# Performance work log

Measured on AMD Instinct MI355X. Metric: run time of the kernel, lower is better.

## Reference

```python
import jax, jax.numpy as jnp
import numpy as np

M_SLOTS, H, W = 10, 88, 88
B, C = 32, 256

def _xavier_normal(key, shape):
    # torch.nn.init.xavier_normal_ for a 3D tensor [M,H,W]:
    # fan_in = H*W (prod of dims after first? torch: fan_in = shape[1]*receptive, fan_out = shape[0]*receptive)
    # For a 3D tensor torch treats dim1=H as fan dims with receptive field W:
    fan_in = shape[1] * shape[2]
    fan_out = shape[0] * shape[2]
    std = float(np.sqrt(2.0 / (fan_in + fan_out)))
    return jax.random.normal(key, shape, dtype=jnp.float32) * std

def setup_inputs() -> dict:
    key = jax.random.key(0)
    kx, km = jax.random.split(key)
    x = jax.random.normal(kx, (B, C, H, W), dtype=jnp.float32)
    mem = _xavier_normal(km, (M_SLOTS, H, W))
    return {"x": x, "mem": mem}

def reference(x, mem):
    # score[b,c,m] = sum_hw x[b,c,h,w] * mem[m,h,w]
    score = jnp.einsum('bchw,mhw->bcm', x, mem)
    score = jax.nn.softmax(score, axis=-1)
    # value[b,c,h,w] = sum_m score[b,c,m] * mem[m,h,w]
    value = jnp.einsum('bcm,mhw->bchw', score, mem)
    return value
```

## Files before the change

### kernel.cpp

```cpp
#include <hip/hip_runtime.h>


#define RROWS   4
#define NM      10
#define NVEC    1936
#define THREADS 256

typedef float f32x4 __attribute__((ext_vector_type(4)));

__global__ __launch_bounds__(THREADS)
void memaug_kernel(const float* __restrict__ x,
                   const float* __restrict__ mem,
                   float* __restrict__ out)
{
    const int tid = threadIdx.x;
    const long r0 = (long)blockIdx.x * RROWS;

    const f32x4* __restrict__ m4  = (const f32x4*)mem;
    const f32x4* __restrict__ xr  = (const f32x4*)x + r0 * NVEC;
    f32x4* __restrict__ orow      = (f32x4*)out + r0 * NVEC;

    float acc[RROWS][NM];
#pragma unroll
    for (int j = 0; j < RROWS; ++j)
#pragma unroll
        for (int m = 0; m < NM; ++m) acc[j][m] = 0.f;

    for (int iv = tid; iv < NVEC; iv += THREADS) {
        f32x4 xv[RROWS];
#pragma unroll
        for (int j = 0; j < RROWS; ++j)
            xv[j] = xr[j * NVEC + iv];
        f32x4 mv[NM];
#pragma unroll
        for (int m = 0; m < NM; ++m)
            mv[m] = m4[m * NVEC + iv];
#pragma unroll
        for (int m = 0; m < NM; ++m) {
#pragma unroll
            for (int j = 0; j < RROWS; ++j) {
                acc[j][m] += xv[j].x * mv[m].x + xv[j].y * mv[m].y
                           + xv[j].z * mv[m].z + xv[j].w * mv[m].w;
            }
        }
    }

#pragma unroll
    for (int j = 0; j < RROWS; ++j)
#pragma unroll
        for (int m = 0; m < NM; ++m) {
            float v = acc[j][m];
#pragma unroll
            for (int off = 32; off > 0; off >>= 1)
                v += __shfl_xor(v, off, 64);
            acc[j][m] = v;
        }

    __shared__ float red[4][RROWS][NM];
    __shared__ float prob[RROWS][NM];

    const int wave = tid >> 6;
    const int lane = tid & 63;
    if (lane == 0) {
#pragma unroll
        for (int j = 0; j < RROWS; ++j)
#pragma unroll
            for (int m = 0; m < NM; ++m) red[wave][j][m] = acc[j][m];
    }
    __syncthreads();

    if (tid < RROWS) {
        const int j = tid;
        float s[NM];
        float mx = -1e30f;
#pragma unroll
        for (int m = 0; m < NM; ++m) {
            s[m] = red[0][j][m] + red[1][j][m] + red[2][j][m] + red[3][j][m];
            mx = fmaxf(mx, s[m]);
        }
        float sum = 0.f;
#pragma unroll
        for (int m = 0; m < NM; ++m) { s[m] = expf(s[m] - mx); sum += s[m]; }
        const float inv = 1.f / sum;
#pragma unroll
        for (int m = 0; m < NM; ++m) prob[j][m] = s[m] * inv;
    }
    __syncthreads();

    float p[RROWS][NM];
#pragma unroll
    for (int j = 0; j < RROWS; ++j)
#pragma unroll
        for (int m = 0; m < NM; ++m) p[j][m] = prob[j][m];

    for (int iv = tid; iv < NVEC; iv += THREADS) {
        f32x4 mv[NM];
#pragma unroll
        for (int m = 0; m < NM; ++m)
            mv[m] = m4[m * NVEC + iv];

        f32x4 ov[RROWS];
#pragma unroll
        for (int j = 0; j < RROWS; ++j) ov[j] = (f32x4)(0.f);
#pragma unroll
        for (int m = 0; m < NM; ++m) {
#pragma unroll
            for (int j = 0; j < RROWS; ++j) {
                ov[j].x += p[j][m] * mv[m].x;
                ov[j].y += p[j][m] * mv[m].y;
                ov[j].z += p[j][m] * mv[m].z;
                ov[j].w += p[j][m] * mv[m].w;
            }
        }
#pragma unroll
        for (int j = 0; j < RROWS; ++j)
            __builtin_nontemporal_store(ov[j], &orow[j * NVEC + iv]);
    }
}

extern "C" void kernel_launch(void* const* d_in, const int* in_sizes, int n_in,
                              void* d_out, int out_size, void* d_ws, size_t ws_size,
                              hipStream_t stream) {
    const float* x   = (const float*)d_in[0];
    const float* mem = (const float*)d_in[1];
    float* out       = (float*)d_out;

    const int rows   = 32 * 256;
    const int blocks = rows / RROWS;

    memaug_kernel<<<blocks, THREADS, 0, stream>>>(x, mem, out);
}
```

Baseline: 88.45 us.

## Assign rows per wave and add per-chunk block barriers to keep waves in lockstep

Each wave now owns two rows and reduces across the full row on its own, so the shared-memory reduction and softmax barriers are gone. A block covers eight rows, and each of the four waves loads the same mem chunk at the same time. A __syncthreads after every chunk keeps the waves aligned so those shared mem reads can hit in cache together. The cost is a barrier on every iteration and a tail guard in the last chunk.

Result: slower. 106.7 us (+20.7%).

```diff
diff --git a/kernel.cpp b/kernel.cpp
--- a/kernel.cpp
+++ b/kernel.cpp
@@ -1,9 +1,12 @@
 #include <hip/hip_runtime.h>
 
 
-#define RROWS   4
+#define RPW     2
+#define NWAVES  4
+#define ROWS_PB (RPW * NWAVES)
 #define NM      10
 #define NVEC    1936
+#define NCHUNK  31
 #define THREADS 256
 
 typedef float f32x4 __attribute__((ext_vector_type(4)));
@@ -13,40 +16,50 @@
                    const float* __restrict__ mem,
                    float* __restrict__ out)
 {
-    const int tid = threadIdx.x;
-    const long r0 = (long)blockIdx.x * RROWS;
+    const int tid  = threadIdx.x;
+    const int lane = tid & 63;
+    const int wv   = tid >> 6;
+    const long rowbase = (long)blockIdx.x * ROWS_PB + (long)wv * RPW;
 
-    const f32x4* __restrict__ m4  = (const f32x4*)mem;
-    const f32x4* __restrict__ xr  = (const f32x4*)x + r0 * NVEC;
-    f32x4* __restrict__ orow      = (f32x4*)out + r0 * NVEC;
+    const f32x4* __restrict__ m4 = (const f32x4*)mem;
+    const f32x4* __restrict__ xr = (const f32x4*)x + rowbase * NVEC;
+    f32x4* __restrict__ orow     = (f32x4*)out + rowbase * NVEC;
 
-    float acc[RROWS][NM];
+    float acc[RPW][NM];
 #pragma unroll
-    for (int j = 0; j < RROWS; ++j)
+    for (int j = 0; j < RPW; ++j)
 #pragma unroll
         for (int m = 0; m < NM; ++m) acc[j][m] = 0.f;
 
-    for (int iv = tid; iv < NVEC; iv += THREADS) {
-        f32x4 xv[RROWS];
+    for (int c = 0; c < NCHUNK; ++c) {
+        const int iv = c * 64 + lane;
+        const bool ok = iv < NVEC;
+
+        f32x4 xv[RPW], mv[NM];
+        if (ok) {
 #pragma unroll
-        for (int j = 0; j < RROWS; ++j)
-            xv[j] = xr[j * NVEC + iv];
-        f32x4 mv[NM];
+            for (int j = 0; j < RPW; ++j)
+                xv[j] = xr[j * NVEC + iv];
 #pragma unroll
-        for (int m = 0; m < NM; ++m)
-            mv[m] = m4[m * NVEC + iv];
+            for (int m = 0; m < NM; ++m)
+                mv[m] = m4[m * NVEC + iv];
+        } else {
+#pragma unroll
+            for (int j = 0; j < RPW; ++j) xv[j] = (f32x4)(0.f);
+        }
 #pragma unroll
         for (int m = 0; m < NM; ++m) {
 #pragma unroll
-            for (int j = 0; j < RROWS; ++j) {
+            for (int j = 0; j < RPW; ++j) {
                 acc[j][m] += xv[j].x * mv[m].x + xv[j].y * mv[m].y
                            + xv[j].z * mv[m].z + xv[j].w * mv[m].w;
             }
         }
+        __syncthreads();
     }
 
 #pragma unroll
-    for (int j = 0; j < RROWS; ++j)
+    for (int j = 0; j < RPW; ++j)
 #pragma unroll
         for (int m = 0; m < NM; ++m) {
             float v = acc[j][m];
@@ -56,65 +69,48 @@
             acc[j][m] = v;
         }
 
-    __shared__ float red[4][RROWS][NM];
-    __shared__ float prob[RROWS][NM];
-
-    const int wave = tid >> 6;
-    const int lane = tid & 63;
-    if (lane == 0) {
+    float p[RPW][NM];
 #pragma unroll
-        for (int j = 0; j < RROWS; ++j)
-#pragma unroll
-            for (int m = 0; m < NM; ++m) red[wave][j][m] = acc[j][m];
-    }
-    __syncthreads();
-
-    if (tid < RROWS) {
-        const int j = tid;
-        float s[NM];
+    for (int j = 0; j < RPW; ++j) {
         float mx = -1e30f;
 #pragma unroll
-        for (int m = 0; m < NM; ++m) {
-            s[m] = red[0][j][m] + red[1][j][m] + red[2][j][m] + red[3][j][m];
-            mx = fmaxf(mx, s[m]);
-        }
+        for (int m = 0; m < NM; ++m) mx = fmaxf(mx, acc[j][m]);
         float sum = 0.f;
 #pragma unroll
-        for (int m = 0; m < NM; ++m) { s[m] = expf(s[m] - mx); sum += s[m]; }
+        for (int m = 0; m < NM; ++m) { p[j][m] = expf(acc[j][m] - mx); sum += p[j][m]; }
         const float inv = 1.f / sum;
 #pragma unroll
-        for (int m = 0; m < NM; ++m) prob[j][m] = s[m] * inv;
+        for (int m = 0; m < NM; ++m) p[j][m] *= inv;
     }
-    __syncthreads();
 
-    float p[RROWS][NM];
+    for (int c = 0; c < NCHUNK; ++c) {
+        const int iv = c * 64 + lane;
+        const bool ok = iv < NVEC;
+
+        if (ok) {
+            f32x4 mv[NM];
 #pragma unroll
-    for (int j = 0; j < RROWS; ++j)
+            for (int m = 0; m < NM; ++m)
+                mv[m] = m4[m * NVEC + iv];
+
+            f32x4 ov[RPW];
 #pragma unroll
-        for (int m = 0; m < NM; ++m) p[j][m] = prob[j][m];
-
-    for (int iv = tid; iv < NVEC; iv += THREADS) {
-        f32x4 mv[NM];
+            for (int j = 0; j < RPW; ++j) ov[j] = (f32x4)(0.f);
 #pragma unroll
-        for (int m = 0; m < NM; ++m)
-            mv[m] = m4[m * NVEC + iv];
-
-        f32x4 ov[RROWS];
+            for (int m = 0; m < NM; ++m) {
 #pragma unroll
-        for (int j = 0; j < RROWS; ++j) ov[j] = (f32x4)(0.f);
+                for (int j = 0; j < RPW; ++j) {
+                    ov[j].x += p[j][m] * mv[m].x;
+                    ov[j].y += p[j][m] * mv[m].y;
+                    ov[j].z += p[j][m] * mv[m].z;
+                    ov[j].w += p[j][m] * mv[m].w;
+                }
+            }
 #pragma unroll
-        for (int m = 0; m < NM; ++m) {
-#pragma unroll
-            for (int j = 0; j < RROWS; ++j) {
-                ov[j].x += p[j][m] * mv[m].x;
-                ov[j].y += p[j][m] * mv[m].y;
-                ov[j].z += p[j][m] * mv[m].z;
-                ov[j].w += p[j][m] * mv[m].w;
-            }
+            for (int j = 0; j < RPW; ++j)
+                __builtin_nontemporal_store(ov[j], &orow[j * NVEC + iv]);
         }
-#pragma unroll
-        for (int j = 0; j < RROWS; ++j)
-            __builtin_nontemporal_store(ov[j], &orow[j * NVEC + iv]);
+        __syncthreads();
     }
 }
 
@@ -126,7 +122,7 @@
     float* out       = (float*)d_out;
 
     const int rows   = 32 * 256;
-    const int blocks = rows / RROWS;
+    const int blocks = rows / ROWS_PB;
 
     memaug_kernel<<<blocks, THREADS, 0, stream>>>(x, mem, out);
 }
```
